# Performance work log

Hardware: AMD Instinct MI355X
Metric: run time of the kernel (lower is better)

## Reference

```python
import jax, jax.numpy as jnp
import numpy as np

K_LO, K_HI = 5, 3
HAM_LO = jnp.asarray(np.outer(np.hamming(K_LO), np.hamming(K_LO)), dtype=jnp.float32)
HAM_HI = jnp.asarray(np.outer(np.hamming(K_HI), np.hamming(K_HI)), dtype=jnp.float32)


def conv2d(x, w, b, pad):
    y = jax.lax.conv_general_dilated(x, w, (1, 1), [(pad, pad), (pad, pad)],
                                     dimension_numbers=('NCHW', 'OIHW', 'NCHW'))
    return y + b[None, :, None, None]


def kernel_normalizer(mask, k, ham):
    # softmax over k*k, modulate by hamming window, renormalize to sum 1
    n, mc, h, w = mask.shape
    ch = mc // (k * k)
    m = jax.nn.softmax(mask.reshape(n, ch, k * k, h, w), axis=2)
    m = m.reshape(n, ch, k, k, h, w) * ham[None, None, :, :, None, None]
    m = m / m.sum(axis=(2, 3), keepdims=True)
    return m.reshape(n, mc, h, w)


def extract_patches(x, k):
    # (n,c,h,w) -> (n,c,k*k,h,w), zero-padded, row-major kernel order (matches CARAFE)
    n, c, h, w = x.shape
    p = k // 2
    xp = jnp.pad(x, ((0, 0), (0, 0), (p, p), (p, p)))
    return jnp.stack([xp[:, :, i:i + h, j:j + w] for i in range(k) for j in range(k)], axis=2)


def carafe(x, mask, k, group, up):
    # content-aware reassembly: mask is at (h*up, w*up); source pixel = out_pixel // up
    n, c, h, w = x.shape
    cg = c // group
    patches = extract_patches(x, k).reshape(n, group, cg, k * k, h, w)
    if up == 1:
        m = mask.reshape(n, group, k * k, h, w)
        return jnp.einsum('ngckhw,ngkhw->ngchw', patches, m).reshape(n, c, h, w)
    m = mask.reshape(n, group, k * k, h, up, w, up)
    out = jnp.einsum('ngckhw,ngkhuwv->ngchuwv', patches, m)
    return out.reshape(n, c, h * up, w * up)


def _forward(hr_feat, lr_feat, W_hr, b_hr, W_lr, b_lr, W_enc, b_enc, W_enc2, b_enc2):
    chf = conv2d(hr_feat, W_hr, b_hr, 0)
    clf = conv2d(lr_feat, W_lr, b_lr, 0)
    mask_hr_hr = conv2d(chf, W_enc2, b_enc2, 1)
    m_hi = kernel_normalizer(mask_hr_hr, K_HI, HAM_HI)
    chf = 2.0 * chf - carafe(chf, m_hi, K_HI, 1, 1)
    mask_lr_hr = conv2d(chf, W_enc, b_enc, 1)
    m_lo = kernel_normalizer(mask_lr_hr, K_LO, HAM_LO)
    # carafe(up=2) output is already at hr resolution -> F.interpolate(nearest) is identity
    mask_lr_lr = carafe(conv2d(clf, W_enc, b_enc, 1), m_lo, K_LO, 1, 2)
    mask_lr = mask_lr_hr + mask_lr_lr
    m_lo2 = kernel_normalizer(mask_lr, K_LO, HAM_LO)
    mask_hr_lr = carafe(conv2d(clf, W_enc2, b_enc2, 1), m_lo2, K_LO, 1, 2)
    mask_hr = mask_hr_hr + mask_hr_lr
    mask_lr_n = kernel_normalizer(mask_lr, K_LO, HAM_LO)
    lr_out = carafe(lr_feat, mask_lr_n, K_LO, 1, 2)
    mask_hr_n = kernel_normalizer(mask_hr, K_HI, HAM_HI)
    hr_out = 2.0 * hr_feat - carafe(hr_feat, mask_hr_n, K_HI, 1, 1)
    return (mask_lr_n, hr_out, lr_out)


def setup_inputs() -> dict:
    key = jax.random.key(0)
    ks = jax.random.split(key, 10)
    B, CHR, CLR, CC = 2, 256, 256, 64
    H, W = 128, 128
    h, w = H // 2, W // 2
    f32 = jnp.float32
    return {
        'hr_feat': jax.random.normal(ks[0], (B, CHR, H, W), f32),
        'lr_feat': jax.random.normal(ks[1], (B, CLR, h, w), f32),
        'W_hr': jax.random.normal(ks[2], (CC, CHR, 1, 1), f32) * 0.05,
        'b_hr': jnp.zeros((CC,), f32),
        'W_lr': jax.random.normal(ks[3], (CC, CLR, 1, 1), f32) * 0.05,
        'b_lr': jnp.zeros((CC,), f32),
        'W_enc': jax.random.normal(ks[4], (K_LO * K_LO, CC, 3, 3), f32) * 0.001,
        'b_enc': jnp.zeros((K_LO * K_LO,), f32),
        'W_enc2': jax.random.normal(ks[5], (K_HI * K_HI, CC, 3, 3), f32) * 0.001,
        'b_enc2': jnp.zeros((K_HI * K_HI,), f32),
    }


def reference(hr_feat, lr_feat, W_hr, b_hr, W_lr, b_lr, W_enc, b_enc, W_enc2, b_enc2):
    return _forward(hr_feat, lr_feat, W_hr, b_hr, W_lr, b_lr, W_enc, b_enc, W_enc2, b_enc2)
```

## Files before the change

kernel.cpp:

```cpp
#include <hip/hip_runtime.h>

#define HWH 16384
#define HWL 4096
#define WH 128
#define WL 64

__device__ __forceinline__ float ham3v(int t) {
    const float h[3] = {0.08f, 1.0f, 0.08f};
    return h[t / 3] * h[t % 3];
}
__device__ __forceinline__ float ham5v(int t) {
    const float h[5] = {0.08f, 0.54f, 1.0f, 0.54f, 0.08f};
    return h[t / 5] * h[t % 5];
}

template <int K>
__device__ __forceinline__ void normalize_post(float* m) {
    constexpr int K2 = K * K;
    float mx = -1e30f;
#pragma unroll
    for (int k = 0; k < K2; k++) mx = fmaxf(mx, m[k]);
    float s = 0.f;
#pragma unroll
    for (int k = 0; k < K2; k++) {
        float hv = (K == 3) ? ham3v(k) : ham5v(k);
        float e = __expf(m[k] - mx) * hv;
        m[k] = e;
        s += e;
    }
    float inv = 1.f / s;
#pragma unroll
    for (int k = 0; k < K2; k++) m[k] *= inv;
}

template <int K>
__device__ __forceinline__ void normalize_mask(const float* __restrict src, int stride,
                                               float* m) {
#pragma unroll
    for (int k = 0; k < K * K; k++) m[k] = src[(size_t)k * stride];
    normalize_post<K>(m);
}

struct F4 { float x, y, z, w; };
__device__ __forceinline__ F4 ld4u(const float* p) {
    F4 v;
    __builtin_memcpy(&v, p, 16);
    return v;
}

__device__ __forceinline__ float4 add4(float4 a, float4 b) {
    return make_float4(a.x + b.x, a.y + b.y, a.z + b.z, a.w + b.w);
}

__global__ void prep_w_k(const float* __restrict Whr, const float* __restrict Wlr,
                         const float* __restrict Wenc, const float* __restrict Wenc2,
                         float* __restrict wbase) {
    int tid = blockIdx.x * blockDim.x + threadIdx.x;
    int stride = gridDim.x * blockDim.x;
    float* wt_hr = wbase;
    float* wt_lr = wbase + 16384;
    float* wtE = wbase + 32768;
    float* wtE2 = wbase + 51200;
    for (int i = tid; i < 16384; i += stride) {
        int ci = i >> 6, co = i & 63;
        wt_hr[i] = Whr[co * 256 + ci];
        wt_lr[i] = Wlr[co * 256 + ci];
    }
    for (int i = tid; i < 18432; i += stride) {
        int r = i >> 5, co = i & 31;
        int ci = r / 9, t = r % 9;
        wtE[i] = (co < 25) ? Wenc[(co * 64 + ci) * 9 + t] : 0.f;
    }
    for (int i = tid; i < 9216; i += stride) {
        int r = i >> 4, co = i & 15;
        int ci = r / 9, t = r % 9;
        wtE2[i] = (co < 9) ? Wenc2[(co * 64 + ci) * 9 + t] : 0.f;
    }
}

__global__ __launch_bounds__(256) void conv1x1_all_k(
    const float* __restrict hr, const float* __restrict lrf, const float* __restrict wt_hr,
    const float* __restrict wt_lr, const float* __restrict bhr, const float* __restrict blr,
    float* __restrict chf, float* __restrict clf, int N) {
    __shared__ float sm[128 * 64];
    int b = blockIdx.x;
    const int HRB = (HWH / 64) * N;
    const float *x, *wt, *bias;
    float* y;
    int HWp, n, px0;
    if (b < HRB) {
        x = hr; wt = wt_hr; bias = bhr; y = chf; HWp = HWH;
        n = b / (HWH / 64);
        px0 = (b % (HWH / 64)) * 64;
    } else {
        int b2 = b - HRB;
        x = lrf; wt = wt_lr; bias = blr; y = clf; HWp = HWL;
        n = b2 / (HWL / 64);
        px0 = (b2 % (HWL / 64)) * 64;
    }
    const float* xb = x + (size_t)n * 256 * HWp + px0;
    int pl = threadIdx.x & 63;
    int co0 = __builtin_amdgcn_readfirstlane((int)(threadIdx.x >> 6)) * 16;
    float acc[16];
#pragma unroll
    for (int j = 0; j < 16; j++) acc[j] = 0.f;
    const float* w0 = wt + co0;
#pragma unroll
    for (int half = 0; half < 2; half++) {
        __syncthreads();
        for (int e = threadIdx.x; e < 2048; e += 256) {
            int ci = e >> 4, q = e & 15;
            *reinterpret_cast<float4*>(sm + ci * 64 + q * 4) =
                *reinterpret_cast<const float4*>(xb + (size_t)(half * 128 + ci) * HWp + q * 4);
        }
        __syncthreads();
        const float* wh = w0 + (half * 128) * 64;
#pragma unroll 8
        for (int ci = 0; ci < 128; ci++) {
            float xv = sm[ci * 64 + pl];
            const float* wr = wh + ci * 64;
#pragma unroll
            for (int j = 0; j < 16; j++) acc[j] = fmaf(wr[j], xv, acc[j]);
        }
    }
    float* yb = y + ((size_t)(n * 64 + co0)) * HWp + px0 + pl;
#pragma unroll
    for (int j = 0; j < 16; j++) yb[(size_t)j * HWp] = acc[j] + bias[co0 + j];
}

template <int COUT, int CH, int PAD, int LOG2W, int HH, int WW, int NCI>
__device__ __forceinline__ void conv3x3_2px(const float* __restrict x,
                                            const float* __restrict wt,
                                            const float* __restrict bias,
                                            float* __restrict y, int n, int g, int pxh,
                                            int ci0, bool addb) {
    constexpr int HWp = HH * WW;
    int px = pxh * 2;
    int yy = px >> LOG2W, xx = px & (WW - 1);
    int co0 = g * CH;
    float a0[CH], a1[CH];
#pragma unroll
    for (int j = 0; j < CH; j++) { a0[j] = 0.f; a1[j] = 0.f; }
    const float* xb = x + (size_t)(n * 64 + ci0) * HWp;
    const float* wb0 = wt + (size_t)ci0 * 9 * PAD + co0;
    int roff[3];
    bool rv[3];
#pragma unroll
    for (int r = 0; r < 3; r++) {
        int sy = yy + r - 1;
        rv[r] = (sy >= 0) && (sy < HH);
        roff[r] = sy * WW + xx - 1;
    }
    bool lv = (xx > 0), rgv = (xx < WW - 2);
    for (int ci = 0; ci < NCI; ci++) {
        const float* xc = xb + (size_t)ci * HWp;
        const float* w = wb0 + (size_t)ci * 9 * PAD;
#pragma unroll
        for (int r = 0; r < 3; r++) {
            F4 v = ld4u(xc + roff[r]);
            float t0 = (rv[r] && lv) ? v.x : 0.f;
            float t1 = rv[r] ? v.y : 0.f;
            float t2 = rv[r] ? v.z : 0.f;
            float t3 = (rv[r] && rgv) ? v.w : 0.f;
#pragma unroll
            for (int j = 0; j < CH; j++) {
                float w0 = w[(r * 3 + 0) * PAD + j];
                float w1 = w[(r * 3 + 1) * PAD + j];
                float w2 = w[(r * 3 + 2) * PAD + j];
                a0[j] = fmaf(w0, t0, fmaf(w1, t1, fmaf(w2, t2, a0[j])));
                a1[j] = fmaf(w0, t1, fmaf(w1, t2, fmaf(w2, t3, a1[j])));
            }
        }
    }
#pragma unroll
    for (int j = 0; j < CH; j++) {
        int co = co0 + j;
        if (co < COUT) {
            float bv = addb ? bias[co] : 0.f;
            float* op = y + ((size_t)(n * COUT + co)) * HWp + px;
            *reinterpret_cast<float2*>(op) = make_float2(a0[j] + bv, a1[j] + bv);
        }
    }
}

__global__ __launch_bounds__(256) void conv3x3_CGK_k(
    const float* __restrict chf, const float* __restrict clf, const float* __restrict wtE,
    const float* __restrict wtE2, const float* __restrict benc,
    const float* __restrict benc2, float* __restrict mh_P, float* __restrict g_P,
    float* __restrict k_P, int N) {
    const size_t MS = (size_t)N * 9 * HWH, GS = (size_t)N * 25 * HWL,
                 KS = (size_t)N * 9 * HWL;
    const int GBl = 8 * N * 5 * 4, KBl = 8 * N * 2 * 4;
    int b = blockIdx.x;
    if (b < GBl) {
        int pxb = b % 8;
        int n = (b / 8) % N;
        int t = b / (8 * N);
        int g = t % 5, s = t / 5;
        conv3x3_2px<25, 5, 32, 6, WL, WL, 16>(clf, wtE, benc, g_P + s * GS, n, g,
                                              pxb * 256 + (int)threadIdx.x, s * 16, s == 0);
    } else if (b < GBl + KBl) {
        int b2 = b - GBl;
        int pxb = b2 % 8;
        int n = (b2 / 8) % N;
        int t = b2 / (8 * N);
        int g = t % 2, s = t / 2;
        conv3x3_2px<9, 5, 16, 6, WL, WL, 16>(clf, wtE2, benc2, k_P + s * KS, n, g,
                                             pxb * 256 + (int)threadIdx.x, s * 16, s == 0);
    } else {
        int b3 = b - GBl - KBl;
        int pxb = b3 % 32;
        int n = (b3 / 32) % N;
        int t = b3 / (32 * N);
        int g = t % 3, s = t / 3;
        conv3x3_2px<9, 3, 16, 7, WH, WH, 16>(chf, wtE2, benc2, mh_P + s * MS, n, g,
                                             pxb * 256 + (int)threadIdx.x, s * 16, s == 0);
    }
}

__global__ __launch_bounds__(256) void conv3x3_F_k(const float* __restrict chf2,
                                                   const float* __restrict wtE,
                                                   const float* __restrict benc,
                                                   float* __restrict mlr_P, int N) {
    const size_t FS = (size_t)N * 25 * HWH;
    int t = blockIdx.x;
    int pxb = t % 32; t /= 32;
    int n = t % N; t /= N;
    int g = t % 5;
    int s = t / 5;
    conv3x3_2px<25, 5, 32, 7, WH, WH, 16>(chf2, wtE, benc, mlr_P + s * FS, n, g,
                                          pxb * 256 + (int)threadIdx.x, s * 16, s == 0);
}

__global__ void sum4_gkc_k(const float4* __restrict mh, float4* __restrict mh_d,
                           const float4* __restrict g, float4* __restrict g_d,
                           const float4* __restrict k, float4* __restrict k_d, int N) {
    const int E1 = N * 9 * HWH / 4, E2 = N * 25 * HWL / 4, E3 = N * 9 * HWL / 4;
    int i = blockIdx.x * 256 + threadIdx.x;
    if (i < E1) {
        mh_d[i] = add4(add4(mh[i], mh[i + E1]), add4(mh[i + 2 * E1], mh[i + 3 * E1]));
    } else if (i < E1 + E2) {
        int j = i - E1;
        g_d[j] = add4(add4(g[j], g[j + E2]), add4(g[j + 2 * E2], g[j + 3 * E2]));
    } else if (i < E1 + E2 + E3) {
        int j = i - E1 - E2;
        k_d[j] = add4(add4(k[j], k[j + E3]), add4(k[j + 2 * E3], k[j + 3 * E3]));
    }
}

__global__ void sum4_f_k(const float4* __restrict p, float4* __restrict d, int N) {
    const int E = N * 25 * HWH / 4;
    int i = blockIdx.x * 256 + threadIdx.x;
    if (i < E) d[i] = add4(add4(p[i], p[i + E]), add4(p[i + 2 * E], p[i + 3 * E]));
}

__global__ void norm9_k(const float* __restrict src, float* __restrict dst, int N) {
    int b = blockIdx.x;
    int px = (b % 256) * 64 + threadIdx.x;
    int n = b / 256;
    float m[9];
    normalize_mask<3>(src + (size_t)n * 9 * HWH + px, HWH, m);
    float* dp = dst + (size_t)n * 9 * HWH + px;
#pragma unroll
    for (int k = 0; k < 9; k++) dp[(size_t)k * HWH] = m[k];
}

template <int NCH>
__device__ __forceinline__ void stage_tile136(const float* __restrict src,
                                              float (*__restrict tile)[10][136], int y0) {
    int tid = threadIdx.x;
    if (tid < 80) {
        int r = tid >> 3, c8 = tid & 7;
        int col = (c8 < 4) ? c8 : 128 + c8;
#pragma unroll
        for (int c = 0; c < NCH; c++) tile[c][r][col] = 0.f;
    }
    int r0 = tid >> 5, q0 = tid & 31;
    int gy0 = y0 + r0 - 1;
    bool v0 = (gy0 >= 0) && (gy0 < WH);
    int e1 = tid + 256;
    int r1 = e1 >> 5, q1 = e1 & 31;
    int gy1 = e1 < 320 ? (y0 + r1 - 1) : 0;
    bool v1 = (e1 < 320) && (y0 + r1 - 1 >= 0) && (y0 + r1 - 1 < WH);
#pragma unroll
    for (int c = 0; c < NCH; c++) {
        const float* sp = src + (size_t)c * HWH;
        float4 a = make_float4(0.f, 0.f, 0.f, 0.f);
        if (v0) a = *(const float4*)(sp + gy0 * WH + q0 * 4);
        *(float4*)&tile[c][r0][4 + q0 * 4] = a;
        if (e1 < 320) {
            float4 bb = make_float4(0.f, 0.f, 0.f, 0.f);
            if (v1) bb = *(const float4*)(sp + gy1 * WH + q1 * 4);
            *(float4*)&tile[c][r1][4 + q1 * 4] = bb;
        }
    }
    __syncthreads();
}

template <int NCH, bool SUBTRACT>
__device__ __forceinline__ void carafe3_tile(const float (*__restrict tile)[10][136],
                                             const float* __restrict mb, int y0,
                                             float* __restrict ob) {
    int ly = threadIdx.x >> 5;
    int x0 = (threadIdx.x & 31) * 4;
    int px = (y0 + ly) * WH + x0;
    float4 m4[9];
#pragma unroll
    for (int t = 0; t < 9; t++) m4[t] = *(const float4*)(mb + (size_t)t * HWH + px);
    for (int c = 0; c < NCH; c++) {
        float row[3][6];
#pragma unroll
        for (int r = 0; r < 3; r++) {
            float lft = tile[c][ly + r][3 + x0];
            float4 mid = *(const float4*)&tile[c][ly + r][4 + x0];
            float rgt = tile[c][ly + r][8 + x0];
            row[r][0] = lft; row[r][1] = mid.x; row[r][2] = mid.y; row[r][3] = mid.z;
            row[r][4] = mid.w; row[r][5] = rgt;
        }
        float4 res;
        float* rp = &res.x;
#pragma unroll
        for (int p = 0; p < 4; p++) {
            float s = 0.f;
#pragma unroll
            for (int r = 0; r < 3; r++)
#pragma unroll
                for (int cc = 0; cc < 3; cc++)
                    s = fmaf(((const float*)&m4[r * 3 + cc])[p], row[r][p + cc], s);
            rp[p] = SUBTRACT ? (2.f * row[1][p + 1] - s) : s;
        }
        *(float4*)(ob + (size_t)c * HWH + px) = res;
    }
}

__global__ __launch_bounds__(256) void fuse_de_k(const float* __restrict chf,
                                                 const float* __restrict m9n,
                                                 float* __restrict chf2, int N) {
    __shared__ float tile[8][10][136];
    int b = blockIdx.x;
    int yt = b & 15;
    int g = (b >> 4) & 7;
    int n = b >> 7;
    int y0 = yt * 8;
    int c0 = g * 8;
    stage_tile136<8>(chf + ((size_t)n * 64 + c0) * HWH, tile, y0);
    carafe3_tile<8, true>(tile, m9n + (size_t)n * 9 * HWH, y0,
                          chf2 + ((size_t)n * 64 + c0) * HWH);
}

__global__ void fuse_hi_k(const float* __restrict m, const float* __restrict g,
                          float* __restrict mask_lr, int N) {
    int b = blockIdx.x;
    int pxb = b % 64;
    int n = (b / 64) % N;
    int co0 = (b / (64 * N)) * 5;
    int px = pxb * 256 + threadIdx.x;
    int Y = px >> 7, X = px & 127;
    int h = Y >> 1, w = X >> 1;
    const float* mb = m + (size_t)n * 25 * HWH + px;
    float ml[25];
    normalize_mask<5>(mb, HWH, ml);
    float acc[5];
#pragma unroll
    for (int j = 0; j < 5; j++) acc[j] = 0.f;
    const float* gb = g + ((size_t)n * 25 + co0) * HWL;
    for (int k = 0; k < 25; k++) {
        int sy = h + k / 5 - 2, sx = w + k % 5 - 2;
        if (sy >= 0 && sy < WL && sx >= 0 && sx < WL) {
            int off = sy * WL + sx;
            float mk = ml[k];
#pragma unroll
            for (int j = 0; j < 5; j++)
                acc[j] = fmaf(mk, gb[(size_t)j * HWL + off], acc[j]);
        }
    }
#pragma unroll
    for (int j = 0; j < 5; j++)
        mask_lr[((size_t)(n * 25 + co0 + j)) * HWH + px] =
            mb[(size_t)(co0 + j) * HWH] + acc[j];
}

__global__ void norm25_k(const float* __restrict mask_lr, float* __restrict out0, int N) {
    int b = blockIdx.x;
    int pxb = b % 256;
    int n = b / 256;
    int px = pxb * 64 + threadIdx.x;
    float m[25];
    normalize_mask<5>(mask_lr + (size_t)n * 25 * HWH + px, HWH, m);
#pragma unroll
    for (int k = 0; k < 25; k++) out0[((size_t)(n * 25 + k)) * HWH + px] = m[k];
}

__global__ void fuse_l_k(const float* __restrict m_n, const float* __restrict kf,
                         const float* __restrict mh, float* __restrict mask_hr, int N) {
    int b = blockIdx.x;
    int pxb = b % 64;
    int n = (b / 64) % N;
    int co0 = (b / (64 * N)) * 3;
    int px = pxb * 256 + threadIdx.x;
    int Y = px >> 7, X = px & 127;
    int h = Y >> 1, w = X >> 1;
    float m[25];
#pragma unroll
    for (int k = 0; k < 25; k++) m[k] = m_n[((size_t)(n * 25 + k)) * HWH + px];
    float acc[3];
#pragma unroll
    for (int j = 0; j < 3; j++) acc[j] = 0.f;
    const float* kb = kf + ((size_t)n * 9 + co0) * HWL;
    for (int k = 0; k < 25; k++) {
        int sy = h + k / 5 - 2, sx = w + k % 5 - 2;
        if (sy >= 0 && sy < WL && sx >= 0 && sx < WL) {
            int off = sy * WL + sx;
            float mk = m[k];
#pragma unroll
            for (int j = 0; j < 3; j++)
                acc[j] = fmaf(mk, kb[(size_t)j * HWL + off], acc[j]);
        }
    }
#pragma unroll
    for (int j = 0; j < 3; j++)
        mask_hr[((size_t)(n * 9 + co0 + j)) * HWH + px] =
            mh[((size_t)(n * 9 + co0 + j)) * HWH + px] + acc[j];
}

#define HRCHG 8
__global__ __launch_bounds__(256) void hr_out_k(const float* __restrict m9n,
                                                const float* __restrict hr,
                                                float* __restrict out1, int N) {
    __shared__ float tile[HRCHG][10][136];
    int b = blockIdx.x;
    int yt = b & 15;
    int g = (b >> 4) & 31;
    int n = b >> 9;
    int y0 = yt * 8;
    int c0 = g * HRCHG;
    stage_tile136<HRCHG>(hr + ((size_t)n * 256 + c0) * HWH, tile, y0);
    carafe3_tile<HRCHG, true>(tile, m9n + (size_t)n * 9 * HWH, y0,
                              out1 + ((size_t)n * 256 + c0) * HWH);
}

#define LRCHG 16
__global__ __launch_bounds__(256, 1) void lr_out_k(const float* __restrict m_n,
                                                   const float* __restrict lr,
                                                   float* __restrict out2, int N) {
    __shared__ float tile[LRCHG][12][68];
    int b = blockIdx.x;
    int yt = b & 7;
    int g = (b >> 3) & 15;
    int n = b >> 7;
    int y0 = yt * 16;
    int hbase = y0 >> 1;
    int c0 = g * LRCHG;
    const float* lrb = lr + ((size_t)n * 256 + c0) * HWL;
    if (threadIdx.x < 48) {
        int r = threadIdx.x >> 2, c4 = threadIdx.x & 3;
        int col = (c4 < 2) ? c4 : 64 + c4;
#pragma unroll
        for (int c = 0; c < LRCHG; c++) tile[c][r][col] = 0.f;
    }
#pragma unroll
    for (int c = 0; c < LRCHG; c++) {
        const float* sp = lrb + (size_t)c * HWL;
#pragma unroll
        for (int p = 0; p < 2; p++) {
            int e = threadIdx.x + p * 256;
            if (e < 384) {
                int r = e >> 5, q = e & 31;
                int h = hbase + r - 2;
                float2 v = make_float2(0.f, 0.f);
                if (h >= 0 && h < WL) v = *(const float2*)(sp + h * WL + q * 2);
                *(float2*)&tile[c][r][2 + q * 2] = v;
            }
        }
    }
    __syncthreads();
    const float* mb = m_n + (size_t)n * 25 * HWH;
    float* ob = out2 + ((size_t)n * 256 + c0) * HWH;
#pragma unroll
    for (int i = 0; i < 2; i++) {
        int q = threadIdx.x + 256 * i;
        int qy = q >> 6, qx = q & 63;
        int Y0 = y0 + 2 * qy;
        int X0 = 2 * qx;
        float2 mk0[25], mk1[25];
#pragma unroll
        for (int k = 0; k < 25; k++) {
            mk0[k] = *(const float2*)(mb + (size_t)k * HWH + Y0 * WH + X0);
            mk1[k] = *(const float2*)(mb + (size_t)k * HWH + (Y0 + 1) * WH + X0);
        }
        for (int c = 0; c < LRCHG; c++) {
            float a00 = 0.f, a01 = 0.f, a10 = 0.f, a11 = 0.f;
#pragma unroll
            for (int k = 0; k < 25; k++) {
                float v = tile[c][qy + k / 5][qx + k % 5];
                a00 = fmaf(mk0[k].x, v, a00);
                a01 = fmaf(mk0[k].y, v, a01);
                a10 = fmaf(mk1[k].x, v, a10);
                a11 = fmaf(mk1[k].y, v, a11);
            }
            float* op = ob + (size_t)c * HWH + (size_t)Y0 * WH + X0;
            *(float2*)op = make_float2(a00, a01);
            *(float2*)(op + WH) = make_float2(a10, a11);
        }
    }
}

extern "C" void kernel_launch(void* const* d_in, const int* in_sizes, int n_in, void* d_out,
                              int out_size, void* d_ws, size_t ws_size, hipStream_t stream) {
    const float* hr = (const float*)d_in[0];
    const float* lr = (const float*)d_in[1];
    const float* Whr = (const float*)d_in[2];
    const float* bhr = (const float*)d_in[3];
    const float* Wlr = (const float*)d_in[4];
    const float* blr = (const float*)d_in[5];
    const float* Wenc = (const float*)d_in[6];
    const float* benc = (const float*)d_in[7];
    const float* Wenc2 = (const float*)d_in[8];
    const float* benc2 = (const float*)d_in[9];
    float* out = (float*)d_out;
    const int B = in_sizes[0] / (256 * HWH);
    (void)d_ws; (void)ws_size;

    float* out0 = out;
    float* O1 = out + (size_t)B * 25 * HWH;
    float* O2 = O1 + (size_t)B * 256 * HWH;

    const size_t MS = (size_t)B * 9 * HWH;
    const size_t GS = (size_t)B * 25 * HWL;
    const size_t KS = (size_t)B * 9 * HWL;
    const size_t FS = (size_t)B * 25 * HWH;

    float* wbase = O2;
    float* wt_hr = wbase;
    float* wt_lr = wbase + 16384;
    float* wtE = wbase + 32768;
    float* wtE2 = wbase + 51200;
    float* mh_P = O2 + 60416;
    float* g_P = mh_P + 4 * MS;
    float* k_P = g_P + 4 * GS;
    float* m_hrhr_sum = k_P + 4 * KS;
    float* g_sum = m_hrhr_sum + MS;
    float* k_sum = g_sum + GS;
    float* m_lrhr_sum = k_sum + KS;
    float* mask_hr = m_lrhr_sum + FS;
    float* mask_hr_n = mask_hr + MS;

    float* chf = O1;
    float* chf2 = chf + (size_t)B * 64 * HWH;
    float* clf = chf2 + (size_t)B * 64 * HWH;
    float* mlr_P = clf + (size_t)B * 64 * HWL;
    float* m_hrhr_n = mlr_P + 4 * FS;
    float* mask_lr = mlr_P;

    prep_w_k<<<64, 256, 0, stream>>>(Whr, Wlr, Wenc, Wenc2, wbase);
    conv1x1_all_k<<<(HWH / 64) * B + (HWL / 64) * B, 256, 0, stream>>>(
        hr, lr, wt_hr, wt_lr, bhr, blr, chf, clf, B);
    conv3x3_CGK_k<<<8 * B * 5 * 4 + 8 * B * 2 * 4 + 32 * B * 3 * 4, 256, 0, stream>>>(
        chf, clf, wtE, wtE2, benc, benc2, mh_P, g_P, k_P, B);
    {
        int e = (int)(MS + GS + KS) / 4;
        sum4_gkc_k<<<(e + 255) / 256, 256, 0, stream>>>(
            (const float4*)mh_P, (float4*)m_hrhr_sum, (const float4*)g_P, (float4*)g_sum,
            (const float4*)k_P, (float4*)k_sum, B);
    }
    norm9_k<<<256 * B, 64, 0, stream>>>(m_hrhr_sum, m_hrhr_n, B);
    fuse_de_k<<<B * 128, 256, 0, stream>>>(chf, m_hrhr_n, chf2, B);
    conv3x3_F_k<<<32 * B * 5 * 4, 256, 0, stream>>>(chf2, wtE, benc, mlr_P, B);
    sum4_f_k<<<((int)FS / 4 + 255) / 256, 256, 0, stream>>>((const float4*)mlr_P,
                                                            (float4*)m_lrhr_sum, B);
    fuse_hi_k<<<64 * B * 5, 256, 0, stream>>>(m_lrhr_sum, g_sum, mask_lr, B);
    norm25_k<<<256 * B, 64, 0, stream>>>(mask_lr, out0, B);
    fuse_l_k<<<64 * B * 3, 256, 0, stream>>>(out0, k_sum, m_hrhr_sum, mask_hr, B);
    norm9_k<<<256 * B, 64, 0, stream>>>(mask_hr, mask_hr_n, B);
    hr_out_k<<<B * 512, 256, 0, stream>>>(mask_hr_n, hr, O1, B);
    lr_out_k<<<B * 128, 256, 0, stream>>>(out0, lr, O2, B);
}
```

Measured before the change: 166.5 us.

## Split conv1x1 input channels across blocks and halve lr_out channel group

```diff
diff --git a/kernel.cpp b/kernel.cpp
--- a/kernel.cpp
+++ b/kernel.cpp
@@ -81,51 +81,66 @@
 __global__ __launch_bounds__(256) void conv1x1_all_k(
     const float* __restrict hr, const float* __restrict lrf, const float* __restrict wt_hr,
     const float* __restrict wt_lr, const float* __restrict bhr, const float* __restrict blr,
-    float* __restrict chf, float* __restrict clf, int N) {
+    float* __restrict chf, float* __restrict clf, float* __restrict chf_pB,
+    float* __restrict clf_pB, int N) {
     __shared__ float sm[128 * 64];
-    int b = blockIdx.x;
+    const int HALF = (HWH / 64) * N + (HWL / 64) * N;
+    int b = blockIdx.x;
+    int s = (b >= HALF) ? 1 : 0;
+    if (s) b -= HALF;
     const int HRB = (HWH / 64) * N;
     const float *x, *wt, *bias;
     float* y;
     int HWp, n, px0;
     if (b < HRB) {
-        x = hr; wt = wt_hr; bias = bhr; y = chf; HWp = HWH;
+        x = hr; wt = wt_hr; bias = bhr; HWp = HWH;
+        y = s ? chf_pB : chf;
         n = b / (HWH / 64);
         px0 = (b % (HWH / 64)) * 64;
     } else {
         int b2 = b - HRB;
-        x = lrf; wt = wt_lr; bias = blr; y = clf; HWp = HWL;
+        x = lrf; wt = wt_lr; bias = blr; HWp = HWL;
+        y = s ? clf_pB : clf;
         n = b2 / (HWL / 64);
         px0 = (b2 % (HWL / 64)) * 64;
     }
-    const float* xb = x + (size_t)n * 256 * HWp + px0;
+    int ci0 = s * 128;
+    const float* xb = x + ((size_t)n * 256 + ci0) * HWp + px0;
     int pl = threadIdx.x & 63;
     int co0 = __builtin_amdgcn_readfirstlane((int)(threadIdx.x >> 6)) * 16;
+    for (int e = threadIdx.x; e < 2048; e += 256) {
+        int ci = e >> 4, q = e & 15;
+        *reinterpret_cast<float4*>(sm + ci * 64 + q * 4) =
+            *reinterpret_cast<const float4*>(xb + (size_t)ci * HWp + q * 4);
+    }
+    __syncthreads();
     float acc[16];
 #pragma unroll
     for (int j = 0; j < 16; j++) acc[j] = 0.f;
-    const float* w0 = wt + co0;
-#pragma unroll
-    for (int half = 0; half < 2; half++) {
-        __syncthreads();
-        for (int e = threadIdx.x; e < 2048; e += 256) {
-            int ci = e >> 4, q = e & 15;
-            *reinterpret_cast<float4*>(sm + ci * 64 + q * 4) =
-                *reinterpret_cast<const float4*>(xb + (size_t)(half * 128 + ci) * HWp + q * 4);
-        }
-        __syncthreads();
-        const float* wh = w0 + (half * 128) * 64;
+    const float* wh = wt + (size_t)ci0 * 64 + co0;
 #pragma unroll 8
-        for (int ci = 0; ci < 128; ci++) {
-            float xv = sm[ci * 64 + pl];
-            const float* wr = wh + ci * 64;
-#pragma unroll
-            for (int j = 0; j < 16; j++) acc[j] = fmaf(wr[j], xv, acc[j]);
-        }
+    for (int ci = 0; ci < 128; ci++) {
+        float xv = sm[ci * 64 + pl];
+        const float* wr = wh + ci * 64;
+#pragma unroll
+        for (int j = 0; j < 16; j++) acc[j] = fmaf(wr[j], xv, acc[j]);
     }
     float* yb = y + ((size_t)(n * 64 + co0)) * HWp + px0 + pl;
 #pragma unroll
-    for (int j = 0; j < 16; j++) yb[(size_t)j * HWp] = acc[j] + bias[co0 + j];
+    for (int j = 0; j < 16; j++)
+        yb[(size_t)j * HWp] = acc[j] + (s ? 0.f : bias[co0 + j]);
+}
+
+__global__ void sum_ab_k(float4* __restrict chf, const float4* __restrict chfB,
+                         float4* __restrict clf, const float4* __restrict clfB, int N) {
+    const int E1 = N * 64 * HWH / 4, E2 = N * 64 * HWL / 4;
+    int i = blockIdx.x * 256 + threadIdx.x;
+    if (i < E1) {
+        chf[i] = add4(chf[i], chfB[i]);
+    } else if (i < E1 + E2) {
+        int j = i - E1;
+        clf[j] = add4(clf[j], clfB[j]);
+    }
 }
 
 template <int COUT, int CH, int PAD, int LOG2W, int HH, int WW, int NCI>
@@ -439,15 +454,15 @@
                               out1 + ((size_t)n * 256 + c0) * HWH);
 }
 
-#define LRCHG 16
-__global__ __launch_bounds__(256, 1) void lr_out_k(const float* __restrict m_n,
-                                                   const float* __restrict lr,
-                                                   float* __restrict out2, int N) {
+#define LRCHG 8
+__global__ __launch_bounds__(256) void lr_out_k(const float* __restrict m_n,
+                                                const float* __restrict lr,
+                                                float* __restrict out2, int N) {
     __shared__ float tile[LRCHG][12][68];
     int b = blockIdx.x;
     int yt = b & 7;
-    int g = (b >> 3) & 15;
-    int n = b >> 7;
+    int g = (b >> 3) & 31;
+    int n = b >> 8;
     int y0 = yt * 16;
     int hbase = y0 >> 1;
     int c0 = g * LRCHG;
@@ -544,6 +559,8 @@
     float* m_lrhr_sum = k_sum + KS;
     float* mask_hr = m_lrhr_sum + FS;
     float* mask_hr_n = mask_hr + MS;
+    float* chf_pB = mask_hr_n + MS;
+    float* clf_pB = chf_pB + (size_t)B * 64 * HWH;
 
     float* chf = O1;
     float* chf2 = chf + (size_t)B * 64 * HWH;
@@ -553,8 +570,10 @@
     float* mask_lr = mlr_P;
 
     prep_w_k<<<64, 256, 0, stream>>>(Whr, Wlr, Wenc, Wenc2, wbase);
-    conv1x1_all_k<<<(HWH / 64) * B + (HWL / 64) * B, 256, 0, stream>>>(
-        hr, lr, wt_hr, wt_lr, bhr, blr, chf, clf, B);
+    conv1x1_all_k<<<((HWH / 64) * B + (HWL / 64) * B) * 2, 256, 0, stream>>>(
+        hr, lr, wt_hr, wt_lr, bhr, blr, chf, clf, chf_pB, clf_pB, B);
+    sum_ab_k<<<(B * 64 * (HWH + HWL) / 4 + 255) / 256, 256, 0, stream>>>(
+        (float4*)chf, (const float4*)chf_pB, (float4*)clf, (const float4*)clf_pB, B);
     conv3x3_CGK_k<<<8 * B * 5 * 4 + 8 * B * 2 * 4 + 32 * B * 3 * 4, 256, 0, stream>>>(
         chf, clf, wtE, wtE2, benc, benc2, mh_P, g_P, k_P, B);
     {
@@ -573,5 +592,5 @@
     fuse_l_k<<<64 * B * 3, 256, 0, stream>>>(out0, k_sum, m_hrhr_sum, mask_hr, B);
     norm9_k<<<256 * B, 64, 0, stream>>>(mask_hr, mask_hr_n, B);
     hr_out_k<<<B * 512, 256, 0, stream>>>(mask_hr_n, hr, O1, B);
-    lr_out_k<<<B * 128, 256, 0, stream>>>(out0, lr, O2, B);
-}
+    lr_out_k<<<B * 256, 256, 0, stream>>>(out0, lr, O2, B);
+}
```

Measured after the change: 160.8 us. -3.4%, faster.
